# Performance work log

Measured on AMD Instinct MI355X. Metric: run time of the kernel, lower is better.

Reference implementation:

```python
import jax, jax.numpy as jnp
import numpy as np

B, H, LQ, LK, DK = 4, 8, 256, 256, 64

def setup_inputs() -> dict:
    key = jax.random.key(0)
    ks = jax.random.split(key, 9)
    s = 1.0 / np.sqrt(DK)
    return {
        "q": jax.random.normal(ks[0], (B, H, LQ, DK), jnp.float32),
        "k": jax.random.normal(ks[1], (B, H, LK, DK), jnp.float32),
        "v": jax.random.normal(ks[2], (B, H, LK, DK), jnp.float32),
        "Wq_w": jax.random.uniform(ks[3], (DK, DK), jnp.float32, -s, s),
        "Wq_b": jax.random.uniform(ks[4], (DK,), jnp.float32, -s, s),
        "Wk_w": jax.random.uniform(ks[5], (DK, DK), jnp.float32, -s, s),
        "Wk_b": jax.random.uniform(ks[6], (DK,), jnp.float32, -s, s),
        "vs_w": jax.random.uniform(ks[7], (1, DK), jnp.float32, -s, s),
        "vs_b": jax.random.uniform(ks[8], (1,), jnp.float32, -s, s),
    }

def reference(q, k, v, Wq_w, Wq_b, Wk_w, Wk_b, vs_w, vs_b):
    # Additive (Bahdanau) attention; dropout is identity at eval time.
    qp = jnp.einsum('bhqd,ed->bhqe', q, Wq_w) + Wq_b          # [B,H,Lq,d_k]
    kp = jnp.einsum('bhkd,ed->bhke', k, Wk_w) + Wk_b          # [B,H,Lk,d_k]
    # Broadcast add -> tanh -> linear projection to scalar score
    feat = jnp.tanh(qp[:, :, :, None, :] + kp[:, :, None, :, :])  # [B,H,Lq,Lk,d_k]
    scores = jnp.einsum('bhqkd,d->bhqk', feat, vs_w[0]) + vs_b[0]  # [B,H,Lq,Lk]
    attn = jax.nn.softmax(scores, axis=-1)
    output = jnp.einsum('bhqk,bhkd->bhqd', attn, v)
    return output, attn
```

## Files before the change

kernel.cpp:

```cpp
#include <hip/hip_runtime.h>

#define B_ 4
#define H_ 8
#define LQ_ 256
#define LK_ 256
#define DK_ 64
#define BH_ (B_*H_)
#define NROWS (BH_*LQ_)
#define QT 4

__global__ __launch_bounds__(256) void proj_kernel(
    const float* __restrict__ qin, const float* __restrict__ kin,
    const float* __restrict__ Wq, const float* __restrict__ bq,
    const float* __restrict__ Wk, const float* __restrict__ bk,
    float* __restrict__ qp, float* __restrict__ kp)
{
    const int which = blockIdx.x >> 8;
    const int rb    = (blockIdx.x & 255) * 32;
    const float* in   = which ? kin : qin;
    const float* W    = which ? Wk  : Wq;
    const float* bias = which ? bk  : bq;
    float* out        = which ? kp  : qp;

    __shared__ float in_s[32*68];
    __shared__ float w_s[64*68];
    const int tid = threadIdx.x;

    {
        const float4* g = (const float4*)(in + rb*64);
        #pragma unroll
        for (int p = 0; p < 2; ++p) {
            int f = tid + p*256;
            float4 x = g[f];
            *(float4*)&in_s[(f>>4)*68 + (f&15)*4] = x;
        }
    }
    {
        const float4* g = (const float4*)W;
        #pragma unroll
        for (int p = 0; p < 4; ++p) {
            int f = tid + p*256;
            float4 x = g[f];
            *(float4*)&w_s[(f>>4)*68 + (f&15)*4] = x;
        }
    }
    __syncthreads();

    const int r  = tid >> 3;
    const int gg = tid & 7;
    float acc[8];
    #pragma unroll
    for (int i = 0; i < 8; ++i) acc[i] = 0.f;

    #pragma unroll
    for (int j = 0; j < 16; ++j) {
        float4 x = *(const float4*)&in_s[r*68 + j*4];
        #pragma unroll
        for (int i = 0; i < 8; ++i) {
            float4 w = *(const float4*)&w_s[(gg + i*8)*68 + j*4];
            acc[i] = fmaf(w.x, x.x, acc[i]);
            acc[i] = fmaf(w.y, x.y, acc[i]);
            acc[i] = fmaf(w.z, x.z, acc[i]);
            acc[i] = fmaf(w.w, x.w, acc[i]);
        }
    }
    float* orow = out + (rb + r)*64;
    #pragma unroll
    for (int i = 0; i < 8; ++i) {
        const int e = gg + i*8;
        orow[e] = acc[i] + bias[e];
    }
}

__global__ __launch_bounds__(256) void score_softmax_pv_kernel(
    const float* __restrict__ qp, const float* __restrict__ kp,
    const float* __restrict__ vs_w, const float* __restrict__ vs_b,
    const float* __restrict__ v,
    float* __restrict__ attn, float* __restrict__ out)
{
    const int bh = blockIdx.x >> 6;
    const int qt = blockIdx.x & 63;
    const int t  = threadIdx.x;
    const int lane = t & 63, wid = t >> 6;

    const float C2  = 2.8853900817779268f;
    const float L2E = 1.4426950408889634f;

    __shared__ float qp_s[QT*64];
    __shared__ float vs_s[64];
    __shared__ float reds[QT][4];
    __shared__ float a_s[QT*256];

    if (t < QT*16) {
        float4 x = ((const float4*)(qp + (bh*LQ_ + qt*QT)*64))[t];
        x.x *= C2; x.y *= C2; x.z *= C2; x.w *= C2;
        ((float4*)qp_s)[t] = x;
    } else if (t < QT*16 + 64) {
        vs_s[t - QT*16] = vs_w[t - QT*16];
    }
    __syncthreads();

    float S = vs_b[0];
    #pragma unroll
    for (int j = 0; j < 16; ++j) {
        float4 w = *(const float4*)&vs_s[j*4];
        S += (w.x + w.y) + (w.z + w.w);
    }

    const float4* kg = (const float4*)(kp + (bh*LK_ + t)*64);

    float sc[QT] = {0.f, 0.f, 0.f, 0.f};
    #pragma unroll 1
    for (int quar = 0; quar < 4; ++quar) {
        float4 kr[4];
        #pragma unroll
        for (int j = 0; j < 4; ++j) {
            float4 kv = kg[quar*4 + j];
            kr[j].x = kv.x*C2; kr[j].y = kv.y*C2;
            kr[j].z = kv.z*C2; kr[j].w = kv.w*C2;
        }
        #pragma unroll
        for (int q = 0; q < QT; ++q) {
            float a0 = 0.f, a1 = 0.f;
            #pragma unroll
            for (int j = 0; j < 4; ++j) {
                float4 qv = *(const float4*)&qp_s[q*64 + quar*16 + j*4];
                float4 wv = *(const float4*)&vs_s[quar*16 + j*4];
                float4 kv = kr[j];
                a0 = fmaf(wv.x, __builtin_amdgcn_rcpf(__builtin_amdgcn_exp2f(qv.x+kv.x)+1.f), a0);
                a1 = fmaf(wv.y, __builtin_amdgcn_rcpf(__builtin_amdgcn_exp2f(qv.y+kv.y)+1.f), a1);
                a0 = fmaf(wv.z, __builtin_amdgcn_rcpf(__builtin_amdgcn_exp2f(qv.z+kv.z)+1.f), a0);
                a1 = fmaf(wv.w, __builtin_amdgcn_rcpf(__builtin_amdgcn_exp2f(qv.w+kv.w)+1.f), a1);
            }
            sc[q] += a0 + a1;
        }
    }

    float p[QT];
    #pragma unroll
    for (int q = 0; q < QT; ++q) {
        p[q] = __builtin_amdgcn_exp2f((S - 2.f*sc[q]) * L2E);
        float s = p[q];
        #pragma unroll
        for (int off = 32; off; off >>= 1) s += __shfl_xor(s, off, 64);
        if (lane == 0) reds[q][wid] = s;
    }
    __syncthreads();
    #pragma unroll
    for (int q = 0; q < QT; ++q) {
        float s = (reds[q][0] + reds[q][1]) + (reds[q][2] + reds[q][3]);
        float a = p[q] * __builtin_amdgcn_rcpf(s);
        attn[(bh*LQ_ + qt*QT + q)*LK_ + t] = a;
        a_s[q*256 + t] = a;
    }
    __syncthreads();

    {
        const int q = t >> 6, d = t & 63;
        const float* vb = v + bh*LK_*DK_ + d;
        float acc = 0.f;
        #pragma unroll 4
        for (int k4 = 0; k4 < 64; ++k4) {
            float4 a4 = *(const float4*)&a_s[q*256 + k4*4];
            acc = fmaf(a4.x, vb[(k4*4+0)*64], acc);
            acc = fmaf(a4.y, vb[(k4*4+1)*64], acc);
            acc = fmaf(a4.z, vb[(k4*4+2)*64], acc);
            acc = fmaf(a4.w, vb[(k4*4+3)*64], acc);
        }
        out[(bh*LQ_ + qt*QT + q)*DK_ + d] = acc;
    }
}

extern "C" void kernel_launch(void* const* d_in, const int* in_sizes, int n_in,
                              void* d_out, int out_size, void* d_ws, size_t ws_size,
                              hipStream_t stream) {
    const float* q    = (const float*)d_in[0];
    const float* k    = (const float*)d_in[1];
    const float* v    = (const float*)d_in[2];
    const float* Wq_w = (const float*)d_in[3];
    const float* Wq_b = (const float*)d_in[4];
    const float* Wk_w = (const float*)d_in[5];
    const float* Wk_b = (const float*)d_in[6];
    const float* vs_w = (const float*)d_in[7];
    const float* vs_b = (const float*)d_in[8];

    float* out  = (float*)d_out;
    float* attn = out + B_*H_*LQ_*DK_;
    float* qp   = (float*)d_ws;
    float* kp   = qp + NROWS*64;

    proj_kernel<<<512, 256, 0, stream>>>(q, k, Wq_w, Wq_b, Wk_w, Wk_b, qp, kp);
    score_softmax_pv_kernel<<<BH_*(LQ_/QT), 256, 0, stream>>>(
        qp, kp, vs_w, vs_b, v, attn, out);
}
```

Baseline: 126.3 us.

## Double queries per block and split PV over keys with shared-memory reduction

Raises the number of query rows per block from 4 to 8, which halves the grid and lets each loaded K row be reused across more queries in the tanh score loop. The P·V stage is restructured so each wave handles a quarter of the keys for all 8 queries. Each V value is loaded once and reused across the 8 queries, and the four per-wave partial sums are then reduced through a new shared buffer. The cost is fewer blocks (1024), more registers per thread, extra shared memory and an extra barrier.

After: 136.1 us. 1.08x slower.

```diff
diff --git a/kernel.cpp b/kernel.cpp
--- a/kernel.cpp
+++ b/kernel.cpp
@@ -7,7 +7,7 @@
 #define DK_ 64
 #define BH_ (B_*H_)
 #define NROWS (BH_*LQ_)
-#define QT 4
+#define QT 8
 
 __global__ __launch_bounds__(256) void proj_kernel(
     const float* __restrict__ qin, const float* __restrict__ kin,
@@ -78,8 +78,8 @@
     const float* __restrict__ v,
     float* __restrict__ attn, float* __restrict__ out)
 {
-    const int bh = blockIdx.x >> 6;
-    const int qt = blockIdx.x & 63;
+    const int bh = blockIdx.x >> 5;
+    const int qt = blockIdx.x & 31;
     const int t  = threadIdx.x;
     const int lane = t & 63, wid = t >> 6;
 
@@ -90,6 +90,7 @@
     __shared__ float vs_s[64];
     __shared__ float reds[QT][4];
     __shared__ float a_s[QT*256];
+    __shared__ float p_s[4*QT*64];
 
     if (t < QT*16) {
         float4 x = ((const float4*)(qp + (bh*LQ_ + qt*QT)*64))[t];
@@ -109,7 +110,10 @@
 
     const float4* kg = (const float4*)(kp + (bh*LK_ + t)*64);
 
-    float sc[QT] = {0.f, 0.f, 0.f, 0.f};
+    float sc[QT];
+    #pragma unroll
+    for (int q = 0; q < QT; ++q) sc[q] = 0.f;
+
     #pragma unroll 1
     for (int quar = 0; quar < 4; ++quar) {
         float4 kr[4];
@@ -156,18 +160,37 @@
     __syncthreads();
 
     {
-        const int q = t >> 6, d = t & 63;
-        const float* vb = v + bh*LK_*DK_ + d;
-        float acc = 0.f;
-        #pragma unroll 4
-        for (int k4 = 0; k4 < 64; ++k4) {
-            float4 a4 = *(const float4*)&a_s[q*256 + k4*4];
-            acc = fmaf(a4.x, vb[(k4*4+0)*64], acc);
-            acc = fmaf(a4.y, vb[(k4*4+1)*64], acc);
-            acc = fmaf(a4.z, vb[(k4*4+2)*64], acc);
-            acc = fmaf(a4.w, vb[(k4*4+3)*64], acc);
-        }
-        out[(bh*LQ_ + qt*QT + q)*DK_ + d] = acc;
+        float acc[QT];
+        #pragma unroll
+        for (int q = 0; q < QT; ++q) acc[q] = 0.f;
+        const float* vb = v + (bh*LK_ + wid*64)*DK_ + lane;
+        #pragma unroll 2
+        for (int k4 = 0; k4 < 16; ++k4) {
+            float v0 = vb[(k4*4+0)*64];
+            float v1 = vb[(k4*4+1)*64];
+            float v2 = vb[(k4*4+2)*64];
+            float v3 = vb[(k4*4+3)*64];
+            #pragma unroll
+            for (int q = 0; q < QT; ++q) {
+                float4 a4 = *(const float4*)&a_s[q*256 + wid*64 + k4*4];
+                acc[q] = fmaf(a4.x, v0, acc[q]);
+                acc[q] = fmaf(a4.y, v1, acc[q]);
+                acc[q] = fmaf(a4.z, v2, acc[q]);
+                acc[q] = fmaf(a4.w, v3, acc[q]);
+            }
+        }
+        #pragma unroll
+        for (int q = 0; q < QT; ++q) p_s[wid*512 + q*64 + lane] = acc[q];
+    }
+    __syncthreads();
+    {
+        float* ob = out + (bh*LQ_ + qt*QT)*DK_;
+        #pragma unroll
+        for (int h = 0; h < 2; ++h) {
+            int idx = t + h*256;
+            float s = (p_s[idx] + p_s[512 + idx]) + (p_s[1024 + idx] + p_s[1536 + idx]);
+            ob[idx] = s;
+        }
     }
 }
 
```
